# Optimization experiments

Measured on AMD Instinct MI355X. Metric: run time of the kernel, lower is better.

## Reference

```python
import jax, jax.numpy as jnp
import numpy as np

NEG_BIG = -9e15  # matches torch's -9000000000000000.0 mask value
LEAKY_SLOPE = 0.2  # alpha passed to nn.LeakyReLU


def setup_inputs() -> dict:
    key = jax.random.key(0)
    k1, k2, k3, k4, k5 = jax.random.split(key, 5)
    N, din, de, dout = 500, 100, 200, 100
    return {
        "input_relations": jax.random.normal(k1, (N, din), dtype=jnp.float32),
        "input_entity_embeds": jax.random.normal(k2, (N, N, de), dtype=jnp.float32),
        "relation_adj": jax.random.randint(k3, (N, N), 0, 2, dtype=jnp.int32),
        "a": jax.random.normal(k4, (dout, 2 * din + de), dtype=jnp.float32) * 0.05,
        "a_2": jax.random.normal(k5, (1, dout), dtype=jnp.float32) * 0.05,
    }


def reference(input_relations, input_entity_embeds, relation_adj, a, a_2):
    # Faithful to: a_input[k=(i,j)] = concat(rel_i, rel_j, ent[i,j]); e = a @ a_input
    # We avoid materializing the (N*N, 2*din+de) concat by splitting `a` into the
    # three blocks that hit rel_i, rel_j and ent[i,j] respectively.
    N, din = input_relations.shape
    de = input_entity_embeds.shape[-1]
    a_src = a[:, :din]          # (dout, din) acts on rel_i
    a_dst = a[:, din:2 * din]   # (dout, din) acts on rel_j
    a_ent = a[:, 2 * din:]      # (dout, de)  acts on ent[i,j]

    # e[i, j, o] = a @ concat(rel_i, rel_j, ent_ij)   -> (N, N, dout)
    e = (
        (input_relations @ a_src.T)[:, None, :]
        + (input_relations @ a_dst.T)[None, :, :]
        + jnp.einsum("ijd,od->ijo", input_entity_embeds.reshape(N, N, de), a_ent)
    )

    # scalar score per pair, leaky relu, masked softmax over neighbors j (dim=1)
    e2 = jax.nn.leaky_relu(e @ a_2[0], LEAKY_SLOPE)  # (N, N)
    scores = jnp.where(relation_adj > 0, e2, jnp.float32(NEG_BIG))
    attention = jax.nn.softmax(scores, axis=1)  # (N, N)

    # weighted sum of the score features e (note: original multiplies attention by e,
    # the pre-leakyrelu linear scores, not by a transformed h)
    h_prime = jnp.einsum("ij,ijo->io", attention, e)  # (N, dout)
    return jax.nn.elu(h_prime)  # concat=True branch
```

## Files before the change

kernel.cpp:

```cpp
#include <hip/hip_runtime.h>
#include <stdint.h>
#include <math.h>

#define N     500
#define DIN   100
#define DE    200
#define DOUT  100
#define AROW  (2*DIN + DE)
#define SLOPE 0.2f

#define JCH   2
#define CROWS 250
#define KP    512
#define BK    720
#define DEP   208
#define GZF   104000

typedef __attribute__((ext_vector_type(8)))  short short8;
typedef __attribute__((ext_vector_type(16))) float f32x16;

static __device__ __forceinline__ unsigned short f2bf(float f) {
  union { float f; uint32_t u; } v; v.f = f;
  uint32_t r = (v.u + 0x7FFFu + ((v.u >> 16) & 1u)) >> 16;
  return (unsigned short)r;
}

__global__ __launch_bounds__(256)
void setup_kernel(const float* __restrict__ R, const float* __restrict__ A,
                  const float* __restrict__ a2,
                  float* __restrict__ src, float* __restrict__ ssrc,
                  float* __restrict__ sdst, float* __restrict__ wv,
                  unsigned short* __restrict__ Bcat, unsigned short* __restrict__ Pbuf,
                  float* __restrict__ gsum, float* __restrict__ Zsum) {
  int b = blockIdx.x, t = threadIdx.x;
  if (b < N) {
    int i = b;
    __shared__ float rrow[DIN];
    __shared__ float sred[4];
    if (t < DIN) rrow[t] = R[i * DIN + t];
    if (t < KP - N) Pbuf[i * KP + N + t] = 0;
    __syncthreads();
    int o = -1; bool isSrc = false;
    if (t < DOUT) { o = t; isSrc = true; }
    else if (t >= 128 && t < 128 + DOUT) { o = t - 128; }
    float val = 0.f;
    if (o >= 0) {
      const float* arow = A + o * AROW + (isSrc ? 0 : DIN);
      #pragma unroll 4
      for (int d = 0; d < DIN; ++d) val += rrow[d] * arow[d];
      if (isSrc) src[i * DOUT + o] = val;
      else       Bcat[o * BK + i] = f2bf(val);
    }
    float red = (o >= 0) ? val * a2[o] : 0.f;
    #pragma unroll
    for (int k = 1; k < 64; k <<= 1) red += __shfl_xor(red, k, 64);
    if ((t & 63) == 0) sred[t >> 6] = red;
    __syncthreads();
    if (t == 0)   ssrc[i] = sred[0] + sred[1];
    if (t == 128) sdst[i] = sred[2] + sred[3];
  } else if (b == N) {
    if (t < DE) {
      float s = 0.f;
      for (int o = 0; o < DOUT; ++o) s += A[o * AROW + 2 * DIN + t] * a2[o];
      wv[t] = s;
    }
  } else if (b <= N + DOUT) {
    int o = b - (N + 1);
    if (t < DE) Bcat[o * BK + KP + t] = f2bf(A[o * AROW + 2 * DIN + t]);
    if (t < KP - N) Bcat[o * BK + N + t] = 0;
    if (t >= 32 && t < 32 + (BK - KP - DE)) Bcat[o * BK + KP + DE + (t - 32)] = 0;
  } else if (b <= 702) {
    int off = (b - 601) * 1024 + t * 4;
    if (off < GZF) *(float4*)(gsum + off) = make_float4(0.f, 0.f, 0.f, 0.f);
  } else {
    if (t < 125) *(float4*)(Zsum + t * 4) = make_float4(0.f, 0.f, 0.f, 0.f);
  }
}

__global__ __launch_bounds__(256, 4)
void passA(const float* __restrict__ E, const int* __restrict__ adj,
           const float* __restrict__ ssrcA, const float* __restrict__ sdstA,
           const float* __restrict__ wv,
           unsigned short* __restrict__ Pbuf,
           float* __restrict__ gsum, float* __restrict__ Zsum) {
  __shared__ int list[CROWS + 6];
  __shared__ float bias[CROWS + 6];
  __shared__ int cntS;
  __shared__ float gl[4][200];
  __shared__ float zl[4];

  int bid = blockIdx.x;
  int i = bid >> 1, c = bid & 1;
  int jbeg = c * CROWS;
  int t = threadIdx.x, wid = t >> 6, lane = t & 63;

  if (t == 0) cntS = 0;
  __syncthreads();

  float ssrc_i = ssrcA[i];
  bool active = false;
  if (t < CROWS) active = (adj[(size_t)i * N + jbeg + t] > 0);
  unsigned long long mask = __ballot(active);
  int wbase = 0;
  if (lane == 0 && mask) wbase = atomicAdd(&cntS, __popcll(mask));
  wbase = __shfl(wbase, 0);
  if (active) {
    int slot = wbase + __popcll(mask & ((1ull << lane) - 1ull));
    list[slot] = jbeg + t;
    bias[slot] = ssrc_i + sdstA[jbeg + t];
  } else if (t < CROWS) {
    Pbuf[i * KP + jbeg + t] = 0;
  }
  __syncthreads();
  int cnt = cntS;

  float4 w4 = make_float4(0.f, 0.f, 0.f, 0.f);
  if (lane < 50) w4 = *(const float4*)(wv + lane * 4);
  float4 g = make_float4(0.f, 0.f, 0.f, 0.f);
  float Z = 0.f;
  const float* Erow = E + (size_t)i * N * DE;

  for (int base = wid * 8; base + 7 < cnt; base += 32) {
    int jr[8];
    float bi[8];
    #pragma unroll
    for (int r = 0; r < 8; ++r) { jr[r] = list[base + r]; bi[r] = bias[base + r]; }
    float4 ev[8];
    if (lane < 50) {
      #pragma unroll
      for (int r = 0; r < 8; ++r)
        ev[r] = *(const float4*)(Erow + (size_t)jr[r] * DE + lane * 4);
    } else {
      #pragma unroll
      for (int r = 0; r < 8; ++r) ev[r] = make_float4(0.f, 0.f, 0.f, 0.f);
    }
    float d[8];
    #pragma unroll
    for (int r = 0; r < 8; ++r)
      d[r] = ev[r].x * w4.x + ev[r].y * w4.y + ev[r].z * w4.z + ev[r].w * w4.w;
    #pragma unroll
    for (int k = 1; k < 64; k <<= 1) {
      #pragma unroll
      for (int r = 0; r < 8; ++r) d[r] += __shfl_xor(d[r], k);
    }
    float p[8];
    float zacc = 0.f;
    #pragma unroll
    for (int r = 0; r < 8; ++r) {
      float s = bi[r] + d[r];
      s = s > 0.f ? s : SLOPE * s;
      p[r] = __expf(s);
      zacc += p[r];
    }
    Z += zacc;
    #pragma unroll
    for (int r = 0; r < 8; ++r) {
      g.x += p[r] * ev[r].x; g.y += p[r] * ev[r].y;
      g.z += p[r] * ev[r].z; g.w += p[r] * ev[r].w;
    }
    if (lane == 0) {
      #pragma unroll
      for (int r = 0; r < 8; ++r) Pbuf[i * KP + jr[r]] = f2bf(p[r]);
    }
  }
  for (int idx = (cnt & ~7) + wid; idx < cnt; idx += 4) {
    int j = list[idx];
    float bi = bias[idx];
    float4 ev = make_float4(0.f, 0.f, 0.f, 0.f);
    if (lane < 50) ev = *(const float4*)(Erow + (size_t)j * DE + lane * 4);
    float d = ev.x * w4.x + ev.y * w4.y + ev.z * w4.z + ev.w * w4.w;
    #pragma unroll
    for (int k = 1; k < 64; k <<= 1) d += __shfl_xor(d, k);
    float s = bi + d; s = s > 0.f ? s : SLOPE * s;
    float p = __expf(s);
    Z += p;
    g.x += p * ev.x; g.y += p * ev.y; g.z += p * ev.z; g.w += p * ev.w;
    if (lane == 0) Pbuf[i * KP + j] = f2bf(p);
  }

  if (lane < 50) *(float4*)&gl[wid][lane * 4] = g;
  if (lane == 0) zl[wid] = Z;
  __syncthreads();
  if (t < 200) {
    float s = gl[0][t] + gl[1][t] + gl[2][t] + gl[3][t];
    atomicAdd(gsum + (size_t)i * DEP + t, s);
  }
  if (t == 200) atomicAdd(Zsum + i, zl[0] + zl[1] + zl[2] + zl[3]);
}

__global__ __launch_bounds__(64)
void combine_kernel(const float* __restrict__ src,
                    const unsigned short* __restrict__ Pbuf,
                    const unsigned short* __restrict__ Bcat,
                    const float* __restrict__ gsum,
                    const float* __restrict__ Zsum,
                    float* __restrict__ out) {
  int b = blockIdx.x;
  int i0 = (b >> 2) * 32;
  int ow = b & 3;
  int t = threadIdx.x;
  int c31 = t & 31, hi = t >> 5;
  int o = ow * 32 + c31;
  int arow = i0 + c31; if (arow > N - 1) arow = N - 1;

  const unsigned short* Prow = Pbuf + (size_t)arow * KP;
  const float* grow = gsum + (size_t)arow * DEP;

  f32x16 acc = {};
  #pragma unroll
  for (int ks = 0; ks < 45; ++ks) {
    short8 a, bf;
    if (ks < 32) {
      a = *(const short8*)(Prow + ks * 16 + hi * 8);
    } else {
      int d0 = (ks - 32) * 16 + hi * 8;
      float4 ga = *(const float4*)(grow + d0);
      float4 gb = *(const float4*)(grow + d0 + 4);
      a[0] = (short)f2bf(ga.x); a[1] = (short)f2bf(ga.y);
      a[2] = (short)f2bf(ga.z); a[3] = (short)f2bf(ga.w);
      a[4] = (short)f2bf(gb.x); a[5] = (short)f2bf(gb.y);
      a[6] = (short)f2bf(gb.z); a[7] = (short)f2bf(gb.w);
    }
    if (o < DOUT) bf = *(const short8*)(Bcat + (size_t)o * BK + ks * 16 + hi * 8);
    else { short8 zz = {}; bf = zz; }
    acc = __builtin_amdgcn_mfma_f32_32x32x16_bf16(a, bf, acc, 0, 0, 0);
  }

  if (o < DOUT) {
    #pragma unroll
    for (int r = 0; r < 16; ++r) {
      int row = (r & 3) + 8 * (r >> 2) + 4 * hi;
      int i = i0 + row;
      if (i < N) {
        float h = src[i * DOUT + o] + acc[r] / Zsum[i];
        out[i * DOUT + o] = h > 0.f ? h : expm1f(h);
      }
    }
  }
}

extern "C" void kernel_launch(void* const* d_in, const int* in_sizes, int n_in,
                              void* d_out, int out_size, void* d_ws, size_t ws_size,
                              hipStream_t stream) {
  const float* R   = (const float*)d_in[0];
  const float* E   = (const float*)d_in[1];
  const int*   adj = (const int*)d_in[2];
  const float* A   = (const float*)d_in[3];
  const float* a2  = (const float*)d_in[4];
  float* out = (float*)d_out;

  char* wsb = (char*)d_ws;
  float*          src  = (float*)(wsb + 0);
  float*          ssrc = (float*)(wsb + 200000);
  float*          sdst = (float*)(wsb + 202000);
  float*          wv   = (float*)(wsb + 204000);
  unsigned short* Bcat = (unsigned short*)(wsb + 204800);
  unsigned short* Pbuf = (unsigned short*)(wsb + 348800);
  float*          gsum = (float*)(wsb + 860800);
  float*          Zsum = (float*)(wsb + 1276800);

  setup_kernel<<<704, 256, 0, stream>>>(R, A, a2, src, ssrc, sdst, wv, Bcat, Pbuf, gsum, Zsum);
  passA<<<N * JCH, 256, 0, stream>>>(E, adj, ssrc, sdst, wv, Pbuf, gsum, Zsum);
  combine_kernel<<<64, 64, 0, stream>>>(src, Pbuf, Bcat, gsum, Zsum, out);
}
```

Baseline: 54.86 us.

## Split passA into per-lane score pass and separate weighted-sum pass

```diff
diff --git a/kernel.cpp b/kernel.cpp
--- a/kernel.cpp
+++ b/kernel.cpp
@@ -83,8 +83,10 @@
            const float* __restrict__ wv,
            unsigned short* __restrict__ Pbuf,
            float* __restrict__ gsum, float* __restrict__ Zsum) {
-  __shared__ int list[CROWS + 6];
-  __shared__ float bias[CROWS + 6];
+  __shared__ int   list[CROWS + 8];
+  __shared__ float bias[CROWS + 8];
+  __shared__ float parr[CROWS + 8];
+  __shared__ float wls[200];
   __shared__ int cntS;
   __shared__ float gl[4][200];
   __shared__ float zl[4];
@@ -95,6 +97,7 @@
   int t = threadIdx.x, wid = t >> 6, lane = t & 63;
 
   if (t == 0) cntS = 0;
+  if (t < 200) wls[t] = wv[t];
   __syncthreads();
 
   float ssrc_i = ssrcA[i];
@@ -114,72 +117,63 @@
   __syncthreads();
   int cnt = cntS;
 
-  float4 w4 = make_float4(0.f, 0.f, 0.f, 0.f);
-  if (lane < 50) w4 = *(const float4*)(wv + lane * 4);
+  int per = (cnt + 3) >> 2;
+  int lo = wid * per;
+  int hi = lo + per; if (hi > cnt) hi = cnt;
+  const float* Erow = E + (size_t)i * N * DE;
+
+  float pz = 0.f;
+  {
+    int s = lo + lane;
+    if (s < hi) {
+      int j = list[s];
+      const float* rp = Erow + (size_t)j * DE;
+      float a0 = 0.f, a1 = 0.f, a2v = 0.f, a3 = 0.f;
+      #pragma unroll 10
+      for (int d4 = 0; d4 < 50; ++d4) {
+        float4 ev = *(const float4*)(rp + d4 * 4);
+        float4 wf = *(const float4*)(&wls[d4 * 4]);
+        a0  += ev.x * wf.x; a1 += ev.y * wf.y;
+        a2v += ev.z * wf.z; a3 += ev.w * wf.w;
+      }
+      float sc = bias[s] + ((a0 + a1) + (a2v + a3));
+      sc = sc > 0.f ? sc : SLOPE * sc;
+      pz = __expf(sc);
+      parr[s] = pz;
+      Pbuf[i * KP + j] = f2bf(pz);
+    }
+  }
+  float Zw = pz;
+  #pragma unroll
+  for (int k = 1; k < 64; k <<= 1) Zw += __shfl_xor(Zw, k);
+
   float4 g = make_float4(0.f, 0.f, 0.f, 0.f);
-  float Z = 0.f;
-  const float* Erow = E + (size_t)i * N * DE;
-
-  for (int base = wid * 8; base + 7 < cnt; base += 32) {
-    int jr[8];
-    float bi[8];
-    #pragma unroll
-    for (int r = 0; r < 8; ++r) { jr[r] = list[base + r]; bi[r] = bias[base + r]; }
-    float4 ev[8];
+  int s2 = lo;
+  for (; s2 + 3 < hi; s2 += 4) {
+    int j0 = list[s2], j1 = list[s2 + 1], j2 = list[s2 + 2], j3 = list[s2 + 3];
+    float p0 = parr[s2], p1 = parr[s2 + 1], p2 = parr[s2 + 2], p3 = parr[s2 + 3];
     if (lane < 50) {
-      #pragma unroll
-      for (int r = 0; r < 8; ++r)
-        ev[r] = *(const float4*)(Erow + (size_t)jr[r] * DE + lane * 4);
-    } else {
-      #pragma unroll
-      for (int r = 0; r < 8; ++r) ev[r] = make_float4(0.f, 0.f, 0.f, 0.f);
-    }
-    float d[8];
-    #pragma unroll
-    for (int r = 0; r < 8; ++r)
-      d[r] = ev[r].x * w4.x + ev[r].y * w4.y + ev[r].z * w4.z + ev[r].w * w4.w;
-    #pragma unroll
-    for (int k = 1; k < 64; k <<= 1) {
-      #pragma unroll
-      for (int r = 0; r < 8; ++r) d[r] += __shfl_xor(d[r], k);
-    }
-    float p[8];
-    float zacc = 0.f;
-    #pragma unroll
-    for (int r = 0; r < 8; ++r) {
-      float s = bi[r] + d[r];
-      s = s > 0.f ? s : SLOPE * s;
-      p[r] = __expf(s);
-      zacc += p[r];
-    }
-    Z += zacc;
-    #pragma unroll
-    for (int r = 0; r < 8; ++r) {
-      g.x += p[r] * ev[r].x; g.y += p[r] * ev[r].y;
-      g.z += p[r] * ev[r].z; g.w += p[r] * ev[r].w;
-    }
-    if (lane == 0) {
-      #pragma unroll
-      for (int r = 0; r < 8; ++r) Pbuf[i * KP + jr[r]] = f2bf(p[r]);
-    }
-  }
-  for (int idx = (cnt & ~7) + wid; idx < cnt; idx += 4) {
-    int j = list[idx];
-    float bi = bias[idx];
-    float4 ev = make_float4(0.f, 0.f, 0.f, 0.f);
-    if (lane < 50) ev = *(const float4*)(Erow + (size_t)j * DE + lane * 4);
-    float d = ev.x * w4.x + ev.y * w4.y + ev.z * w4.z + ev.w * w4.w;
-    #pragma unroll
-    for (int k = 1; k < 64; k <<= 1) d += __shfl_xor(d, k);
-    float s = bi + d; s = s > 0.f ? s : SLOPE * s;
-    float p = __expf(s);
-    Z += p;
-    g.x += p * ev.x; g.y += p * ev.y; g.z += p * ev.z; g.w += p * ev.w;
-    if (lane == 0) Pbuf[i * KP + j] = f2bf(p);
+      float4 e0 = *(const float4*)(Erow + (size_t)j0 * DE + lane * 4);
+      float4 e1 = *(const float4*)(Erow + (size_t)j1 * DE + lane * 4);
+      float4 e2 = *(const float4*)(Erow + (size_t)j2 * DE + lane * 4);
+      float4 e3 = *(const float4*)(Erow + (size_t)j3 * DE + lane * 4);
+      g.x += p0 * e0.x + p1 * e1.x + p2 * e2.x + p3 * e3.x;
+      g.y += p0 * e0.y + p1 * e1.y + p2 * e2.y + p3 * e3.y;
+      g.z += p0 * e0.z + p1 * e1.z + p2 * e2.z + p3 * e3.z;
+      g.w += p0 * e0.w + p1 * e1.w + p2 * e2.w + p3 * e3.w;
+    }
+  }
+  for (; s2 < hi; ++s2) {
+    int j = list[s2];
+    float p = parr[s2];
+    if (lane < 50) {
+      float4 ev = *(const float4*)(Erow + (size_t)j * DE + lane * 4);
+      g.x += p * ev.x; g.y += p * ev.y; g.z += p * ev.z; g.w += p * ev.w;
+    }
   }
 
   if (lane < 50) *(float4*)&gl[wid][lane * 4] = g;
-  if (lane == 0) zl[wid] = Z;
+  if (lane == 0) zl[wid] = Zw;
   __syncthreads();
   if (t < 200) {
     float s = gl[0][t] + gl[1][t] + gl[2][t] + gl[3][t];
```

Result: slower. 68.51 us (+24.9%).

## Double-buffer entity-embedding loads in passA and split MFMA accumulators in combine

Applied to the files above, without the earlier changes.

```diff
diff --git a/kernel.cpp b/kernel.cpp
--- a/kernel.cpp
+++ b/kernel.cpp
@@ -77,14 +77,53 @@
   }
 }
 
+#define LOADBUF(EV, BB) do {                                               \
+    if (lane < 50) {                                                       \
+      _Pragma("unroll")                                                    \
+      for (int r = 0; r < 8; ++r) {                                        \
+        int j_ = list[(BB) + r];                                           \
+        EV[r] = *(const float4*)(Erow + (size_t)j_ * DE + lane * 4);       \
+      }                                                                    \
+    }                                                                      \
+  } while (0)
+
+#define COMPUTE(EV, BB) do {                                               \
+    float d_[8];                                                           \
+    _Pragma("unroll")                                                      \
+    for (int r = 0; r < 8; ++r)                                            \
+      d_[r] = EV[r].x * w4.x + EV[r].y * w4.y + EV[r].z * w4.z + EV[r].w * w4.w; \
+    _Pragma("unroll")                                                      \
+    for (int k = 1; k < 64; k <<= 1) {                                     \
+      _Pragma("unroll")                                                    \
+      for (int r = 0; r < 8; ++r) d_[r] += __shfl_xor(d_[r], k);           \
+    }                                                                      \
+    float p_[8]; float za_ = 0.f;                                          \
+    _Pragma("unroll")                                                      \
+    for (int r = 0; r < 8; ++r) {                                          \
+      float s_ = bias[(BB) + r] + d_[r];                                   \
+      s_ = s_ > 0.f ? s_ : SLOPE * s_;                                     \
+      p_[r] = __expf(s_); za_ += p_[r];                                    \
+    }                                                                      \
+    Z += za_;                                                              \
+    _Pragma("unroll")                                                      \
+    for (int r = 0; r < 8; ++r) {                                          \
+      g.x += p_[r] * EV[r].x; g.y += p_[r] * EV[r].y;                      \
+      g.z += p_[r] * EV[r].z; g.w += p_[r] * EV[r].w;                      \
+    }                                                                      \
+    if (lane == 0) {                                                       \
+      _Pragma("unroll")                                                    \
+      for (int r = 0; r < 8; ++r) Pbuf[i * KP + list[(BB) + r]] = f2bf(p_[r]); \
+    }                                                                      \
+  } while (0)
+
 __global__ __launch_bounds__(256, 4)
 void passA(const float* __restrict__ E, const int* __restrict__ adj,
            const float* __restrict__ ssrcA, const float* __restrict__ sdstA,
            const float* __restrict__ wv,
            unsigned short* __restrict__ Pbuf,
            float* __restrict__ gsum, float* __restrict__ Zsum) {
-  __shared__ int list[CROWS + 6];
-  __shared__ float bias[CROWS + 6];
+  __shared__ int list[CROWS + 8];
+  __shared__ float bias[CROWS + 8];
   __shared__ int cntS;
   __shared__ float gl[4][200];
   __shared__ float zl[4];
@@ -120,47 +159,26 @@
   float Z = 0.f;
   const float* Erow = E + (size_t)i * N * DE;
 
-  for (int base = wid * 8; base + 7 < cnt; base += 32) {
-    int jr[8];
-    float bi[8];
-    #pragma unroll
-    for (int r = 0; r < 8; ++r) { jr[r] = list[base + r]; bi[r] = bias[base + r]; }
-    float4 ev[8];
-    if (lane < 50) {
-      #pragma unroll
-      for (int r = 0; r < 8; ++r)
-        ev[r] = *(const float4*)(Erow + (size_t)jr[r] * DE + lane * 4);
-    } else {
-      #pragma unroll
-      for (int r = 0; r < 8; ++r) ev[r] = make_float4(0.f, 0.f, 0.f, 0.f);
-    }
-    float d[8];
-    #pragma unroll
-    for (int r = 0; r < 8; ++r)
-      d[r] = ev[r].x * w4.x + ev[r].y * w4.y + ev[r].z * w4.z + ev[r].w * w4.w;
-    #pragma unroll
-    for (int k = 1; k < 64; k <<= 1) {
-      #pragma unroll
-      for (int r = 0; r < 8; ++r) d[r] += __shfl_xor(d[r], k);
-    }
-    float p[8];
-    float zacc = 0.f;
-    #pragma unroll
-    for (int r = 0; r < 8; ++r) {
-      float s = bi[r] + d[r];
-      s = s > 0.f ? s : SLOPE * s;
-      p[r] = __expf(s);
-      zacc += p[r];
-    }
-    Z += zacc;
-    #pragma unroll
-    for (int r = 0; r < 8; ++r) {
-      g.x += p[r] * ev[r].x; g.y += p[r] * ev[r].y;
-      g.z += p[r] * ev[r].z; g.w += p[r] * ev[r].w;
-    }
-    if (lane == 0) {
-      #pragma unroll
-      for (int r = 0; r < 8; ++r) Pbuf[i * KP + jr[r]] = f2bf(p[r]);
+  float4 evA[8], evB[8];
+  #pragma unroll
+  for (int r = 0; r < 8; ++r) {
+    evA[r] = make_float4(0.f, 0.f, 0.f, 0.f);
+    evB[r] = make_float4(0.f, 0.f, 0.f, 0.f);
+  }
+  int base = wid * 8;
+  if (base + 7 < cnt) {
+    LOADBUF(evA, base);
+    for (;;) {
+      int nb = base + 32;
+      if (nb + 7 < cnt) LOADBUF(evB, nb);
+      COMPUTE(evA, base);
+      base = nb;
+      if (!(base + 7 < cnt)) break;
+      nb = base + 32;
+      if (nb + 7 < cnt) LOADBUF(evA, nb);
+      COMPUTE(evB, base);
+      base = nb;
+      if (!(base + 7 < cnt)) break;
     }
   }
   for (int idx = (cnt & ~7) + wid; idx < cnt; idx += 4) {
@@ -206,7 +224,7 @@
   const unsigned short* Prow = Pbuf + (size_t)arow * KP;
   const float* grow = gsum + (size_t)arow * DEP;
 
-  f32x16 acc = {};
+  f32x16 acc0 = {}, acc1 = {};
   #pragma unroll
   for (int ks = 0; ks < 45; ++ks) {
     short8 a, bf;
@@ -223,7 +241,8 @@
     }
     if (o < DOUT) bf = *(const short8*)(Bcat + (size_t)o * BK + ks * 16 + hi * 8);
     else { short8 zz = {}; bf = zz; }
-    acc = __builtin_amdgcn_mfma_f32_32x32x16_bf16(a, bf, acc, 0, 0, 0);
+    if (ks & 1) acc1 = __builtin_amdgcn_mfma_f32_32x32x16_bf16(a, bf, acc1, 0, 0, 0);
+    else        acc0 = __builtin_amdgcn_mfma_f32_32x32x16_bf16(a, bf, acc0, 0, 0, 0);
   }
 
   if (o < DOUT) {
@@ -232,7 +251,7 @@
       int row = (r & 3) + 8 * (r >> 2) + 4 * hi;
       int i = i0 + row;
       if (i < N) {
-        float h = src[i * DOUT + o] + acc[r] / Zsum[i];
+        float h = src[i * DOUT + o] + (acc0[r] + acc1[r]) / Zsum[i];
         out[i * DOUT + o] = h > 0.f ? h : expm1f(h);
       }
     }
```

Result: slower. 57.03 us (+3.9%).
